# Kernel optimization log

Hardware: AMD Instinct MI355X
Metric: run time of the kernel (lower is better)

The kernel has to match this reference:

```python
import jax, jax.numpy as jnp
import numpy as np

# Tsit5 Butcher tableau (Tsitouras 2011), b7 = 0 for the accepted solution.
_C = (0.161, 0.327, 0.9, 0.9800255409045097, 1.0)
_A = (
    (0.161,),
    (-0.008480655492356989, 0.335480655492357),
    (2.8971530571054935, -6.359448489975075, 4.3622954328695815),
    (5.325864828439257, -11.748883564062828, 7.4955393428898365, -0.09249506636175525),
    (5.86145544294642, -12.92096931784711, 8.159367898576159, -0.071584973281401, -0.028269050394068383),
)
_B = (0.09646076681806523, 0.01, 0.4798896504144996, 1.379008574103742, -3.290069515436081, 2.324710524099774)

K_STEPS, BATCH, N_STATE, N_INPUT, HIDDEN = 512, 64, 128, 32, 256


def setup_inputs() -> dict:
    key = jax.random.key(0)
    k1, k2, k3, k4 = jax.random.split(key, 4)
    ts = jnp.linspace(0.0, 1.0, K_STEPS, dtype=jnp.float32)
    y0 = jax.random.normal(k1, (BATCH, N_STATE), dtype=jnp.float32)
    us = jax.random.normal(k2, (BATCH, K_STEPS, N_INPUT), dtype=jnp.float32)
    fan_in = 1 + N_STATE + N_INPUT  # t, y, u
    W1 = jax.random.normal(k3, (HIDDEN, fan_in), dtype=jnp.float32) / np.sqrt(fan_in)
    b1 = jnp.zeros((HIDDEN,), dtype=jnp.float32)
    W2 = jax.random.normal(k4, (N_STATE, HIDDEN), dtype=jnp.float32) / np.sqrt(HIDDEN)
    b2 = jnp.zeros((N_STATE,), dtype=jnp.float32)
    return {"ts": ts, "y0": y0, "us": us, "W1": W1, "b1": b1, "W2": W2, "b2": b2}


def _solve(ts, y0_i, us_i, W1, b1, W2, b2):
    """Integrate one trajectory with fixed-step Tsit5 on the save grid."""
    dt_grid = jnp.diff(ts)                              # (k-1,)
    # backward-Hermite derivative estimates for the input signal u(t)
    d = jnp.diff(us_i, axis=0) / dt_grid[:, None]       # (k-1, m)
    d = jnp.concatenate([d[:1], d], axis=0)             # (k, m)

    def func(t, y, u):
        z = jnp.concatenate([t[None], y, u])
        return W2 @ jnp.tanh(W1 @ z + b1) + b2

    def u_at(i, theta):
        # cubic Hermite interpolation of u on interval [ts[i], ts[i+1]]
        h = dt_grid[i]
        u0, u1, d0, d1 = us_i[i], us_i[i + 1], d[i], d[i + 1]
        t2 = theta * theta
        t3 = t2 * theta
        return ((2 * t3 - 3 * t2 + 1) * u0 + (t3 - 2 * t2 + theta) * h * d0
                + (-2 * t3 + 3 * t2) * u1 + (t3 - t2) * h * d1)

    def step(y, i):
        t0, h = ts[i], dt_grid[i]
        ks = []
        k = func(t0, y, u_at(i, jnp.float32(0.0)))
        ks.append(k)
        for c, arow in zip(_C, _A):
            ytmp = y + h * sum(a * kj for a, kj in zip(arow, ks))
            ks.append(func(t0 + c * h, ytmp, u_at(i, jnp.float32(c))))
        y_new = y + h * sum(b * kj for b, kj in zip(_B, ks))
        return y_new, y_new

    _, ys = jax.lax.scan(step, y0_i, jnp.arange(ts.shape[0] - 1))
    return jnp.concatenate([y0_i[None], ys], axis=0)    # (k, n)


def reference(ts, y0, us, W1, b1, W2, b2):
    return jax.vmap(_solve, in_axes=(None, 0, 0, None, None, None, None))(
        ts, y0, us, W1, b1, W2, b2
    )
```

## Files before the change

### kernel.cpp

```cpp
#include <hip/hip_runtime.h>

namespace {

typedef _Float16 h2 __attribute__((ext_vector_type(2)));
typedef _Float16 f16x8 __attribute__((ext_vector_type(8)));
typedef float    f32x4 __attribute__((ext_vector_type(4)));

constexpr int KSTEPS = 512;
constexpr int NSTATE = 128;
constexpr int NINPUT = 32;
constexpr int HID    = 256;
constexpr int FANIN  = 161;
constexpr int BATCH  = 64;
constexpr int CHUNK  = 64;
constexpr int NCH    = 8;

constexpr size_t WS_M  = 0;
constexpr size_t WS_C  = WS_M + (size_t)HID * HID * 2;
constexpr size_t WS_US = WS_C + HID * 4;
constexpr size_t WS_HB = WS_US + (size_t)BATCH * KSTEPS * NINPUT * 2;
constexpr size_t WS_T  = WS_HB + (size_t)BATCH * KSTEPS * HID * 2;

__device__ __forceinline__ float fdot2(h2 a, h2 b, float c) {
#if __has_builtin(__builtin_amdgcn_fdot2)
  return __builtin_amdgcn_fdot2(a, b, c, false);
#else
  return c + (float)a[0] * (float)b[0] + (float)a[1] * (float)b[1];
#endif
}

__device__ __forceinline__ float fast_tanh(float x) {
  float e2 = __builtin_amdgcn_exp2f(x * 2.8853900817779268f);
  float r  = __builtin_amdgcn_rcpf(e2 + 1.0f);
  return __builtin_fmaf(-2.0f, r, 1.0f);
}

#define BAR() __asm__ volatile("s_waitcnt lgkmcnt(0)\n\ts_barrier" ::: "memory")

union F4 { float4 f; h2 h[4]; };

__global__ __launch_bounds__(256)
void k1_compose(const float* __restrict__ W1, const float* __restrict__ W2,
                const float* __restrict__ b2, _Float16* __restrict__ wsM,
                float* __restrict__ wsC) {
  const int j  = blockIdx.x;
  const int hc = threadIdx.x;
  const float* w1row = W1 + (size_t)j * FANIN + 1;
  float acc = 0.0f;
  for (int o = 0; o < NSTATE; ++o)
    acc = __builtin_fmaf(w1row[o], W2[(size_t)o * HID + hc], acc);
  wsM[(size_t)j * HID + hc] = (_Float16)acc;
  if (hc == 0) {
    float ca = 0.0f;
    for (int o = 0; o < NSTATE; ++o) ca = __builtin_fmaf(w1row[o], b2[o], ca);
    wsC[j] = ca;
  }
}

__global__ __launch_bounds__(256)
void k1b_transcode(const float* __restrict__ us, _Float16* __restrict__ us16) {
  const size_t idx = ((size_t)blockIdx.x * 256 + threadIdx.x) * 4;
  const float4 v = *(const float4*)(us + idx);
  us16[idx + 0] = (_Float16)v.x;
  us16[idx + 1] = (_Float16)v.y;
  us16[idx + 2] = (_Float16)v.z;
  us16[idx + 3] = (_Float16)v.w;
}

__global__ __launch_bounds__(256)
__attribute__((amdgpu_waves_per_eu(1, 1)))
void k2_main(const float* __restrict__ ts,
             const float* __restrict__ y0,
             const float* __restrict__ W1,
             const float* __restrict__ b1,
             char* __restrict__ ws)
{
  const int lt = threadIdx.x;
  const int w  = lt >> 6;
  const int ln = lt & 63;
  const int klo = ((ln >> 4) & 3) * 8;
  const int j  = 64 * w + 16 * ((ln >> 2) & 3) + 4 * (ln >> 4) + (ln & 3);
  const int b  = blockIdx.x;

  const _Float16* wsM  = (const _Float16*)(ws + WS_M);
  const float*    wsC  = (const float*)(ws + WS_C);
  const _Float16* us16 = (const _Float16*)(ws + WS_US) + (size_t)b * KSTEPS * NINPUT;
  _Float16*       wsHB = (_Float16*)(ws + WS_HB) + (size_t)b * KSTEPS * HID;
  float*          wsT  = (float*)(ws + WS_T) + (size_t)b * NCH * HID;

  __shared__ __align__(16) _Float16 hbuf[2][HID];
  __shared__ __align__(16) float y0s[NSTATE];
  __shared__ __align__(16) float tss[KSTEPS];
  __shared__ __align__(16) _Float16 usl[KSTEPS * NINPUT];

  {
    const F4* src = (const F4*)us16;
    F4* dst = (F4*)usl;
    #pragma unroll
    for (int it = 0; it < 8; ++it) dst[lt + 256 * it] = src[lt + 256 * it];
    tss[lt] = ts[lt];
    tss[lt + 256] = ts[lt + 256];
  }

  f16x8 af[4][8];
  #pragma unroll
  for (int t = 0; t < 4; ++t) {
    const int row = 64 * w + 16 * t + (ln & 15);
    #pragma unroll
    for (int kk = 0; kk < 8; ++kk)
      af[t][kk] = *(const f16x8*)(wsM + (size_t)row * HID + kk * 32 + klo);
  }

  const float* w1row = W1 + (size_t)j * FANIN;
  const float  w1t   = w1row[0];
  h2 w1u[16];
  #pragma unroll
  for (int i = 0; i < 16; ++i)
    w1u[i] = h2{(_Float16)w1row[129 + 2 * i], (_Float16)w1row[130 + 2 * i]};
  const float cR = wsC[j];

  if (lt < NSTATE) y0s[lt] = y0[(size_t)b * NSTATE + lt];
  __syncthreads();
  float P = b1[j];
  {
    const float* wy = w1row + 1;
    #pragma unroll 8
    for (int o = 0; o < NSTATE; ++o) P = __builtin_fmaf(wy[o], y0s[o], P);
  }

  constexpr double CcD[5] = {0.161, 0.327, 0.9, 0.9800255409045097, 1.0};
  constexpr float Af[5][5] = {
    {0.161f, 0.f, 0.f, 0.f, 0.f},
    {-0.008480655492356989f, 0.335480655492357f, 0.f, 0.f, 0.f},
    {2.8971530571054935f, -6.359448489975075f, 4.3622954328695815f, 0.f, 0.f},
    {5.325864828439257f, -11.748883564062828f, 7.4955393428898365f, -0.09249506636175525f, 0.f},
    {5.86145544294642f, -12.92096931784711f, 8.159367898576159f, -0.071584973281401f,
     -0.028269050394068383f}};
  constexpr float Bf[6] = {0.09646076681806523f, 0.01f, 0.4798896504144996f,
                           1.379008574103742f, -3.290069515436081f, 2.324710524099774f};

  float Ua, Ub = 0.0f, Uaprev = 0.0f, D = 0.0f;
  {
    const F4* up = (const F4*)(usl);
    F4 u0 = up[0], u1 = up[1], u2 = up[2], u3 = up[3];
    float s = 0.0f;
    #pragma unroll
    for (int i = 0; i < 4; ++i) {
      s = fdot2(w1u[i],      u0.h[i], s);
      s = fdot2(w1u[4 + i],  u1.h[i], s);
      s = fdot2(w1u[8 + i],  u2.h[i], s);
      s = fdot2(w1u[12 + i], u3.h[i], s);
    }
    Ua = s;
  }

  float tcur = ts[0], tn1 = ts[1];
  float dtp = 1.0f;
  float h0v = fast_tanh(P + Ua + w1t * tcur);
  hbuf[0][j] = (_Float16)h0v;
  float hB = Bf[0] * h0v;
  float Sacc = 0.0f;
  float aR[6];

  for (int i = 0; i < KSTEPS - 1; ++i) {
    const float dt = tn1 - tcur;
    const int   i2 = (i + 2 < KSTEPS) ? (i + 2) : (KSTEPS - 1);
    const float tn2 = tss[i2];
    F4 ur0, ur1, ur2, ur3;
    {
      const F4* up = (const F4*)(&usl[(i + 1) * NINPUT]);
      ur0 = up[0]; ur1 = up[1]; ur2 = up[2]; ur3 = up[3];
    }

    if (i > 0 && (i & (CHUNK - 1)) == 0)
      wsT[(size_t)(i >> 6) * HID + j] = Sacc;

    #pragma unroll
    for (int e = 0; e < 6; ++e) {
      BAR();

      if (e == 5) {
        wsHB[(size_t)i * HID + j] = (_Float16)hB;
      }
      if (e == 0) {
        float s = 0.0f;
        #pragma unroll
        for (int q = 0; q < 4; ++q) {
          s = fdot2(w1u[q],      ur0.h[q], s);
          s = fdot2(w1u[4 + q],  ur1.h[q], s);
          s = fdot2(w1u[8 + q],  ur2.h[q], s);
          s = fdot2(w1u[12 + q], ur3.h[q], s);
        }
        Ub = s;
        D = (i == 0) ? (Ub - Ua)
                     : (Ua - Uaprev) * (dt * __builtin_amdgcn_rcpf(dtp));
      }

      const _Float16* hb = hbuf[e & 1];
      f32x4 ac0 = {0.f, 0.f, 0.f, 0.f};
      f32x4 ac1 = {0.f, 0.f, 0.f, 0.f};
      f32x4 ac2 = {0.f, 0.f, 0.f, 0.f};
      f32x4 ac3 = {0.f, 0.f, 0.f, 0.f};
      #pragma unroll
      for (int kk = 0; kk < 8; ++kk) {
        const f16x8 bf = *(const f16x8*)(hb + kk * 32 + klo);
        ac0 = __builtin_amdgcn_mfma_f32_16x16x32_f16(af[0][kk], bf, ac0, 0, 0, 0);
        ac1 = __builtin_amdgcn_mfma_f32_16x16x32_f16(af[1][kk], bf, ac1, 0, 0, 0);
        ac2 = __builtin_amdgcn_mfma_f32_16x16x32_f16(af[2][kk], bf, ac2, 0, 0, 0);
        ac3 = __builtin_amdgcn_mfma_f32_16x16x32_f16(af[3][kk], bf, ac3, 0, 0, 0);
      }
      float ae;
      {
        const bool b0 = (ln & 1) != 0;
        const bool b1s = (ln & 2) != 0;
        float e0 = b1s ? (b0 ? ac0[3] : ac0[2]) : (b0 ? ac0[1] : ac0[0]);
        float e1 = b1s ? (b0 ? ac1[3] : ac1[2]) : (b0 ? ac1[1] : ac1[0]);
        float e2 = b1s ? (b0 ? ac2[3] : ac2[2]) : (b0 ? ac2[1] : ac2[0]);
        float e3 = b1s ? (b0 ? ac3[3] : ac3[2]) : (b0 ? ac3[1] : ac3[0]);
        const bool t0 = (ln & 4) != 0;
        const bool t1 = (ln & 8) != 0;
        ae = t1 ? (t0 ? e3 : e2) : (t0 ? e1 : e0);
      }
      ae += cR;
      aR[e] = ae;

      if (e < 5) {
        float acm = 0.0f;
        #pragma unroll
        for (int mm = 0; mm <= e; ++mm) acm = __builtin_fmaf(Af[e][mm], aR[mm], acm);
        const double th = CcD[e];
        const float cu0 = (float)(th * th * th - 2.0 * th * th + 1.0);
        const float cu1 = (float)(2.0 * th * th - th * th * th);
        const float cd0 = (float)(th * th * th - 2.0 * th * th + th);
        const float ut  = cu0 * Ua + cu1 * Ub + cd0 * D;
        const float te  = __builtin_fmaf((float)th, dt, tcur);
        float pre = __builtin_fmaf(dt, acm, P) + ut;
        pre = __builtin_fmaf(w1t, te, pre);
        const float hv = fast_tanh(pre);
        hbuf[(e + 1) & 1][j] = (_Float16)hv;
        hB = __builtin_fmaf(Bf[e + 1], hv, hB);
      } else {
        float acm = 0.0f;
        #pragma unroll
        for (int mm = 0; mm < 6; ++mm) acm = __builtin_fmaf(Bf[mm], aR[mm], acm);
        P = __builtin_fmaf(dt, acm, P);
        Sacc = __builtin_fmaf(dt, hB, Sacc);
        float pre = P + Ub;
        pre = __builtin_fmaf(w1t, tn1, pre);
        const float hv = fast_tanh(pre);
        hbuf[0][j] = (_Float16)hv;
        hB = Bf[0] * hv;
      }
    }

    Uaprev = Ua; Ua = Ub;
    dtp = dt; tcur = tn1; tn1 = tn2;
  }
}

__global__ __launch_bounds__(256, 1)
void k4_out(const float* __restrict__ ts,
            const float* __restrict__ y0,
            const float* __restrict__ W2,
            const char* __restrict__ ws,
            float* __restrict__ out)
{
  const int blk = blockIdx.x;
  const int b = blk >> 3;
  const int c = blk & 7;
  const int lt = threadIdx.x;
  const int o    = lt >> 1;
  const int half = lt & 1;

  const _Float16* wsHB = (const _Float16*)(ws + WS_HB) + (size_t)b * KSTEPS * HID;
  const float*    wsT  = (const float*)(ws + WS_T) + (size_t)b * NCH * HID;
  float* outb = out + (size_t)b * KSTEPS * NSTATE;

  __shared__ __align__(16) _Float16 Sb[HID];

  h2 w2r[64];
  {
    const float* row = W2 + (size_t)o * HID + 128 * half;
    #pragma unroll
    for (int i = 0; i < 64; ++i)
      w2r[i] = h2{(_Float16)row[2 * i], (_Float16)row[2 * i + 1]};
  }
  const float y0o = y0[(size_t)b * NSTATE + o];
  if (c == 0 && lt < NSTATE) outb[lt] = y0[(size_t)b * NSTATE + lt];

  float S = (c > 0) ? wsT[(size_t)c * HID + lt] : 0.0f;
  const int i0 = c * CHUNK;
  const int n  = (KSTEPS - 1 - i0 < CHUNK) ? (KSTEPS - 1 - i0) : CHUNK;

  float tc = ts[i0], tn = ts[i0 + 1];
  float hcur = (float)wsHB[(size_t)i0 * HID + lt];
  for (int l = 0; l < n; ++l) {
    const int i = i0 + l;
    const int inx = (i + 1 < KSTEPS - 1) ? (i + 1) : (KSTEPS - 2);
    const float hnext = (float)wsHB[(size_t)inx * HID + lt];
    const float tnn = ts[(i + 2 < KSTEPS) ? (i + 2) : (KSTEPS - 1)];

    const float dt = tn - tc;
    S = __builtin_fmaf(dt, hcur, S);
    Sb[lt] = (_Float16)S;
    __syncthreads();

    const F4* sp = (const F4*)(&Sb[128 * half]);
    float v0 = 0.0f, v1 = 0.0f;
    #pragma unroll
    for (int q = 0; q < 16; ++q) {
      F4 sc = sp[q];
      v0 = fdot2(w2r[4 * q + 0], sc.h[0], v0);
      v1 = fdot2(w2r[4 * q + 1], sc.h[1], v1);
      v0 = fdot2(w2r[4 * q + 2], sc.h[2], v0);
      v1 = fdot2(w2r[4 * q + 3], sc.h[3], v1);
    }
    float v = v0 + v1;
    v += __shfl_xor(v, 1);
    if (half == 0) outb[(size_t)(i + 1) * NSTATE + o] = y0o + v;
    __syncthreads();

    hcur = hnext; tc = tn; tn = tnn;
  }
}

}

extern "C" void kernel_launch(void* const* d_in, const int* in_sizes, int n_in,
                              void* d_out, int out_size, void* d_ws, size_t ws_size,
                              hipStream_t stream) {
  const float* ts = (const float*)d_in[0];
  const float* y0 = (const float*)d_in[1];
  const float* us = (const float*)d_in[2];
  const float* W1 = (const float*)d_in[3];
  const float* b1 = (const float*)d_in[4];
  const float* W2 = (const float*)d_in[5];
  const float* b2 = (const float*)d_in[6];
  float* out = (float*)d_out;
  char* ws = (char*)d_ws;

  _Float16* wsM  = (_Float16*)(ws + WS_M);
  float*    wsC  = (float*)(ws + WS_C);
  _Float16* us16 = (_Float16*)(ws + WS_US);

  hipLaunchKernelGGL(k1_compose, dim3(HID), dim3(HID), 0, stream, W1, W2, b2, wsM, wsC);
  hipLaunchKernelGGL(k1b_transcode, dim3(BATCH * KSTEPS * NINPUT / 1024), dim3(256),
                     0, stream, us, us16);
  hipLaunchKernelGGL(k2_main, dim3(BATCH), dim3(256), 0, stream, ts, y0, W1, b1, ws);
  hipLaunchKernelGGL(k4_out, dim3(BATCH * NCH), dim3(256), 0, stream, ts, y0, W2,
                     (const char*)ws, out);
}
```

Measured before the change: 1.546 ms.

## Split k2_main GEMV across 8 waves with redundant lane pairs per row

Runs the per-trajectory recurrent kernel with 512 threads (8 waves) instead of 256. Each wave now owns 32 hidden rows, issuing two MFMA tiles per kk step instead of four. The output-to-lane mapping is rearranged so each hidden unit is computed by two lanes, and only one of them writes to LDS and global memory. The aim is to shorten the serial MFMA chain per stage, at the cost of more threads doing duplicate scalar tanh work and more waves taking part in each barrier.

```diff
diff --git a/kernel.cpp b/kernel.cpp
--- a/kernel.cpp
+++ b/kernel.cpp
@@ -67,8 +67,8 @@
   us16[idx + 3] = (_Float16)v.w;
 }
 
-__global__ __launch_bounds__(256)
-__attribute__((amdgpu_waves_per_eu(1, 1)))
+__global__ __launch_bounds__(512)
+__attribute__((amdgpu_waves_per_eu(2, 2)))
 void k2_main(const float* __restrict__ ts,
              const float* __restrict__ y0,
              const float* __restrict__ W1,
@@ -78,8 +78,11 @@
   const int lt = threadIdx.x;
   const int w  = lt >> 6;
   const int ln = lt & 63;
-  const int klo = ((ln >> 4) & 3) * 8;
-  const int j  = 64 * w + 16 * ((ln >> 2) & 3) + 4 * (ln >> 4) + (ln & 3);
+  const int c  = ln & 15;
+  const int q  = (ln >> 4) & 3;
+  const int klo = q * 8;
+  const int j  = 32 * w + 16 * (c & 1) + 4 * q + ((c >> 1) & 3);
+  const bool wrl = (c < 8);
   const int b  = blockIdx.x;
 
   const _Float16* wsM  = (const _Float16*)(ws + WS_M);
@@ -97,15 +100,14 @@
     const F4* src = (const F4*)us16;
     F4* dst = (F4*)usl;
     #pragma unroll
-    for (int it = 0; it < 8; ++it) dst[lt + 256 * it] = src[lt + 256 * it];
+    for (int it = 0; it < 4; ++it) dst[lt + 512 * it] = src[lt + 512 * it];
     tss[lt] = ts[lt];
-    tss[lt + 256] = ts[lt + 256];
-  }
-
-  f16x8 af[4][8];
+  }
+
+  f16x8 af[2][8];
   #pragma unroll
-  for (int t = 0; t < 4; ++t) {
-    const int row = 64 * w + 16 * t + (ln & 15);
+  for (int t = 0; t < 2; ++t) {
+    const int row = 32 * w + 16 * t + (ln & 15);
     #pragma unroll
     for (int kk = 0; kk < 8; ++kk)
       af[t][kk] = *(const f16x8*)(wsM + (size_t)row * HID + kk * 32 + klo);
@@ -157,7 +159,7 @@
   float tcur = ts[0], tn1 = ts[1];
   float dtp = 1.0f;
   float h0v = fast_tanh(P + Ua + w1t * tcur);
-  hbuf[0][j] = (_Float16)h0v;
+  if (wrl) hbuf[0][j] = (_Float16)h0v;
   float hB = Bf[0] * h0v;
   float Sacc = 0.0f;
   float aR[6];
@@ -172,24 +174,24 @@
       ur0 = up[0]; ur1 = up[1]; ur2 = up[2]; ur3 = up[3];
     }
 
-    if (i > 0 && (i & (CHUNK - 1)) == 0)
+    if (i > 0 && (i & (CHUNK - 1)) == 0 && wrl)
       wsT[(size_t)(i >> 6) * HID + j] = Sacc;
 
     #pragma unroll
     for (int e = 0; e < 6; ++e) {
       BAR();
 
-      if (e == 5) {
+      if (e == 5 && wrl) {
         wsHB[(size_t)i * HID + j] = (_Float16)hB;
       }
       if (e == 0) {
         float s = 0.0f;
         #pragma unroll
-        for (int q = 0; q < 4; ++q) {
-          s = fdot2(w1u[q],      ur0.h[q], s);
-          s = fdot2(w1u[4 + q],  ur1.h[q], s);
-          s = fdot2(w1u[8 + q],  ur2.h[q], s);
-          s = fdot2(w1u[12 + q], ur3.h[q], s);
+        for (int qq = 0; qq < 4; ++qq) {
+          s = fdot2(w1u[qq],      ur0.h[qq], s);
+          s = fdot2(w1u[4 + qq],  ur1.h[qq], s);
+          s = fdot2(w1u[8 + qq],  ur2.h[qq], s);
+          s = fdot2(w1u[12 + qq], ur3.h[qq], s);
         }
         Ub = s;
         D = (i == 0) ? (Ub - Ua)
@@ -199,27 +201,22 @@
       const _Float16* hb = hbuf[e & 1];
       f32x4 ac0 = {0.f, 0.f, 0.f, 0.f};
       f32x4 ac1 = {0.f, 0.f, 0.f, 0.f};
-      f32x4 ac2 = {0.f, 0.f, 0.f, 0.f};
-      f32x4 ac3 = {0.f, 0.f, 0.f, 0.f};
       #pragma unroll
       for (int kk = 0; kk < 8; ++kk) {
         const f16x8 bf = *(const f16x8*)(hb + kk * 32 + klo);
         ac0 = __builtin_amdgcn_mfma_f32_16x16x32_f16(af[0][kk], bf, ac0, 0, 0, 0);
         ac1 = __builtin_amdgcn_mfma_f32_16x16x32_f16(af[1][kk], bf, ac1, 0, 0, 0);
-        ac2 = __builtin_amdgcn_mfma_f32_16x16x32_f16(af[2][kk], bf, ac2, 0, 0, 0);
-        ac3 = __builtin_amdgcn_mfma_f32_16x16x32_f16(af[3][kk], bf, ac3, 0, 0, 0);
       }
       float ae;
       {
-        const bool b0 = (ln & 1) != 0;
-        const bool b1s = (ln & 2) != 0;
-        float e0 = b1s ? (b0 ? ac0[3] : ac0[2]) : (b0 ? ac0[1] : ac0[0]);
-        float e1 = b1s ? (b0 ? ac1[3] : ac1[2]) : (b0 ? ac1[1] : ac1[0]);
-        float e2 = b1s ? (b0 ? ac2[3] : ac2[2]) : (b0 ? ac2[1] : ac2[0]);
-        float e3 = b1s ? (b0 ? ac3[3] : ac3[2]) : (b0 ? ac3[1] : ac3[0]);
-        const bool t0 = (ln & 4) != 0;
-        const bool t1 = (ln & 8) != 0;
-        ae = t1 ? (t0 ? e3 : e2) : (t0 ? e1 : e0);
+        const bool tsel = (c & 1) != 0;
+        float v0 = tsel ? ac1[0] : ac0[0];
+        float v1 = tsel ? ac1[1] : ac0[1];
+        float v2 = tsel ? ac1[2] : ac0[2];
+        float v3 = tsel ? ac1[3] : ac0[3];
+        const bool r0 = (c & 2) != 0;
+        const bool r1 = (c & 4) != 0;
+        ae = r1 ? (r0 ? v3 : v2) : (r0 ? v1 : v0);
       }
       ae += cR;
       aR[e] = ae;
@@ -237,7 +234,7 @@
         float pre = __builtin_fmaf(dt, acm, P) + ut;
         pre = __builtin_fmaf(w1t, te, pre);
         const float hv = fast_tanh(pre);
-        hbuf[(e + 1) & 1][j] = (_Float16)hv;
+        if (wrl) hbuf[(e + 1) & 1][j] = (_Float16)hv;
         hB = __builtin_fmaf(Bf[e + 1], hv, hB);
       } else {
         float acm = 0.0f;
@@ -248,7 +245,7 @@
         float pre = P + Ub;
         pre = __builtin_fmaf(w1t, tn1, pre);
         const float hv = fast_tanh(pre);
-        hbuf[0][j] = (_Float16)hv;
+        if (wrl) hbuf[0][j] = (_Float16)hv;
         hB = Bf[0] * hv;
       }
     }
@@ -346,7 +343,7 @@
   hipLaunchKernelGGL(k1_compose, dim3(HID), dim3(HID), 0, stream, W1, W2, b2, wsM, wsC);
   hipLaunchKernelGGL(k1b_transcode, dim3(BATCH * KSTEPS * NINPUT / 1024), dim3(256),
                      0, stream, us, us16);
-  hipLaunchKernelGGL(k2_main, dim3(BATCH), dim3(256), 0, stream, ts, y0, W1, b1, ws);
+  hipLaunchKernelGGL(k2_main, dim3(BATCH), dim3(512), 0, stream, ts, y0, W1, b1, ws);
   hipLaunchKernelGGL(k4_out, dim3(BATCH * NCH), dim3(256), 0, stream, ts, y0, W2,
                      (const char*)ws, out);
 }
```

After: 1.591 ms. 1.03x slower.

## Pair two trajectories per block and ping-pong MFMA with scalar stage tails

Applied to the files above, without the earlier changes.

k2_main now runs two batch trajectories per 512-thread block, two waves per SIMD, and launches half as many blocks. The groups are staggered by half a stage: while one group runs the MFMA matvec for the current RK stage, the other computes its tanh/Hermite tail, with a barrier between the phases. The lagging group keeps its hidden state in a register and writes it to shared memory just before its own MFMA. The aim is to hide the serial scalar tail latency behind the other trajectory's matrix work. The cost is two barriers per stage instead of one, and half as many CUs in use.

```diff
diff --git a/kernel.cpp b/kernel.cpp
--- a/kernel.cpp
+++ b/kernel.cpp
@@ -67,20 +67,22 @@
   us16[idx + 3] = (_Float16)v.w;
 }
 
-__global__ __launch_bounds__(256)
-__attribute__((amdgpu_waves_per_eu(1, 1)))
+__global__ __launch_bounds__(512)
+__attribute__((amdgpu_waves_per_eu(2, 2)))
 void k2_main(const float* __restrict__ ts,
              const float* __restrict__ y0,
              const float* __restrict__ W1,
              const float* __restrict__ b1,
              char* __restrict__ ws)
 {
-  const int lt = threadIdx.x;
-  const int w  = lt >> 6;
-  const int ln = lt & 63;
+  const int lt  = threadIdx.x;
+  const int tg  = lt >> 8;
+  const int ltg = lt & 255;
+  const int w   = ltg >> 6;
+  const int ln  = ltg & 63;
   const int klo = ((ln >> 4) & 3) * 8;
-  const int j  = 64 * w + 16 * ((ln >> 2) & 3) + 4 * (ln >> 4) + (ln & 3);
-  const int b  = blockIdx.x;
+  const int j   = 64 * w + 16 * ((ln >> 2) & 3) + 4 * (ln >> 4) + (ln & 3);
+  const int b   = blockIdx.x * 2 + tg;
 
   const _Float16* wsM  = (const _Float16*)(ws + WS_M);
   const float*    wsC  = (const float*)(ws + WS_C);
@@ -88,18 +90,17 @@
   _Float16*       wsHB = (_Float16*)(ws + WS_HB) + (size_t)b * KSTEPS * HID;
   float*          wsT  = (float*)(ws + WS_T) + (size_t)b * NCH * HID;
 
-  __shared__ __align__(16) _Float16 hbuf[2][HID];
-  __shared__ __align__(16) float y0s[NSTATE];
+  __shared__ __align__(16) _Float16 hbuf[2][2][HID];
+  __shared__ __align__(16) float y0s[2][NSTATE];
   __shared__ __align__(16) float tss[KSTEPS];
-  __shared__ __align__(16) _Float16 usl[KSTEPS * NINPUT];
+  __shared__ __align__(16) _Float16 usl[2][KSTEPS * NINPUT];
 
   {
     const F4* src = (const F4*)us16;
-    F4* dst = (F4*)usl;
-    #pragma unroll
-    for (int it = 0; it < 8; ++it) dst[lt + 256 * it] = src[lt + 256 * it];
+    F4* dst = (F4*)usl[tg];
+    #pragma unroll
+    for (int it = 0; it < 8; ++it) dst[ltg + 256 * it] = src[ltg + 256 * it];
     tss[lt] = ts[lt];
-    tss[lt + 256] = ts[lt + 256];
   }
 
   f16x8 af[4][8];
@@ -119,13 +120,13 @@
     w1u[i] = h2{(_Float16)w1row[129 + 2 * i], (_Float16)w1row[130 + 2 * i]};
   const float cR = wsC[j];
 
-  if (lt < NSTATE) y0s[lt] = y0[(size_t)b * NSTATE + lt];
+  if (ltg < NSTATE) y0s[tg][ltg] = y0[(size_t)b * NSTATE + ltg];
   __syncthreads();
   float P = b1[j];
   {
     const float* wy = w1row + 1;
     #pragma unroll 8
-    for (int o = 0; o < NSTATE; ++o) P = __builtin_fmaf(wy[o], y0s[o], P);
+    for (int o = 0; o < NSTATE; ++o) P = __builtin_fmaf(wy[o], y0s[tg][o], P);
   }
 
   constexpr double CcD[5] = {0.161, 0.327, 0.9, 0.9800255409045097, 1.0};
@@ -141,7 +142,7 @@
 
   float Ua, Ub = 0.0f, Uaprev = 0.0f, D = 0.0f;
   {
-    const F4* up = (const F4*)(usl);
+    const F4* up = (const F4*)(usl[tg]);
     F4 u0 = up[0], u1 = up[1], u2 = up[2], u3 = up[3];
     float s = 0.0f;
     #pragma unroll
@@ -157,10 +158,89 @@
   float tcur = ts[0], tn1 = ts[1];
   float dtp = 1.0f;
   float h0v = fast_tanh(P + Ua + w1t * tcur);
-  hbuf[0][j] = (_Float16)h0v;
+  if (tg == 0) hbuf[0][0][j] = (_Float16)h0v;
+  float hreg = h0v;
   float hB = Bf[0] * h0v;
   float Sacc = 0.0f;
   float aR[6];
+  __syncthreads();
+
+  #define READ_MFMA(EB)                                                        \
+    {                                                                          \
+      const _Float16* hb = hbuf[tg][EB];                                       \
+      f32x4 ac0 = {0.f, 0.f, 0.f, 0.f};                                        \
+      f32x4 ac1 = {0.f, 0.f, 0.f, 0.f};                                        \
+      f32x4 ac2 = {0.f, 0.f, 0.f, 0.f};                                        \
+      f32x4 ac3 = {0.f, 0.f, 0.f, 0.f};                                        \
+      _Pragma("unroll")                                                        \
+      for (int kk = 0; kk < 8; ++kk) {                                         \
+        const f16x8 bf = *(const f16x8*)(hb + kk * 32 + klo);                  \
+        ac0 = __builtin_amdgcn_mfma_f32_16x16x32_f16(af[0][kk], bf, ac0, 0, 0, 0); \
+        ac1 = __builtin_amdgcn_mfma_f32_16x16x32_f16(af[1][kk], bf, ac1, 0, 0, 0); \
+        ac2 = __builtin_amdgcn_mfma_f32_16x16x32_f16(af[2][kk], bf, ac2, 0, 0, 0); \
+        ac3 = __builtin_amdgcn_mfma_f32_16x16x32_f16(af[3][kk], bf, ac3, 0, 0, 0); \
+      }                                                                        \
+      const bool b0 = (ln & 1) != 0;                                           \
+      const bool b1s = (ln & 2) != 0;                                          \
+      float e0 = b1s ? (b0 ? ac0[3] : ac0[2]) : (b0 ? ac0[1] : ac0[0]);        \
+      float e1 = b1s ? (b0 ? ac1[3] : ac1[2]) : (b0 ? ac1[1] : ac1[0]);        \
+      float e2 = b1s ? (b0 ? ac2[3] : ac2[2]) : (b0 ? ac2[1] : ac2[0]);        \
+      float e3 = b1s ? (b0 ? ac3[3] : ac3[2]) : (b0 ? ac3[1] : ac3[0]);        \
+      const bool t0 = (ln & 4) != 0;                                           \
+      const bool t1 = (ln & 8) != 0;                                           \
+      ae = t1 ? (t0 ? e3 : e2) : (t0 ? e1 : e0);                               \
+    }
+
+  #define TAIL(E, DO_W)                                                        \
+    {                                                                          \
+      if ((E) == 0) {                                                          \
+        float s = 0.0f;                                                        \
+        _Pragma("unroll")                                                      \
+        for (int qq = 0; qq < 4; ++qq) {                                       \
+          s = fdot2(w1u[qq],      ur0.h[qq], s);                               \
+          s = fdot2(w1u[4 + qq],  ur1.h[qq], s);                               \
+          s = fdot2(w1u[8 + qq],  ur2.h[qq], s);                               \
+          s = fdot2(w1u[12 + qq], ur3.h[qq], s);                               \
+        }                                                                      \
+        Ub = s;                                                                \
+        D = (i == 0) ? (Ub - Ua)                                               \
+                     : (Ua - Uaprev) * (dt * __builtin_amdgcn_rcpf(dtp));      \
+      }                                                                        \
+      ae += cR;                                                                \
+      aR[(E)] = ae;                                                            \
+      if ((E) < 5) {                                                           \
+        float acm = 0.0f;                                                      \
+        _Pragma("unroll")                                                      \
+        for (int mm = 0; mm <= (E); ++mm)                                      \
+          acm = __builtin_fmaf(Af[(E)][mm], aR[mm], acm);                      \
+        const double th = CcD[(E)];                                            \
+        const float cu0 = (float)(th * th * th - 2.0 * th * th + 1.0);         \
+        const float cu1 = (float)(2.0 * th * th - th * th * th);               \
+        const float cd0 = (float)(th * th * th - 2.0 * th * th + th);          \
+        const float ut  = cu0 * Ua + cu1 * Ub + cd0 * D;                       \
+        const float te  = __builtin_fmaf((float)th, dt, tcur);                 \
+        float pre = __builtin_fmaf(dt, acm, P) + ut;                           \
+        pre = __builtin_fmaf(w1t, te, pre);                                    \
+        const float hv = fast_tanh(pre);                                       \
+        if (DO_W) hbuf[tg][((E) + 1) & 1][j] = (_Float16)hv;                   \
+        else      hreg = hv;                                                   \
+        hB = __builtin_fmaf(Bf[(E) + 1], hv, hB);                              \
+      } else {                                                                 \
+        wsHB[(size_t)i * HID + j] = (_Float16)hB;                              \
+        float acm = 0.0f;                                                      \
+        _Pragma("unroll")                                                      \
+        for (int mm = 0; mm < 6; ++mm)                                         \
+          acm = __builtin_fmaf(Bf[mm], aR[mm], acm);                           \
+        P = __builtin_fmaf(dt, acm, P);                                        \
+        Sacc = __builtin_fmaf(dt, hB, Sacc);                                   \
+        float pre = P + Ub;                                                    \
+        pre = __builtin_fmaf(w1t, tn1, pre);                                   \
+        const float hv = fast_tanh(pre);                                       \
+        if (DO_W) hbuf[tg][0][j] = (_Float16)hv;                               \
+        else      hreg = hv;                                                   \
+        hB = Bf[0] * hv;                                                       \
+      }                                                                        \
+    }
 
   for (int i = 0; i < KSTEPS - 1; ++i) {
     const float dt = tn1 - tcur;
@@ -168,7 +248,7 @@
     const float tn2 = tss[i2];
     F4 ur0, ur1, ur2, ur3;
     {
-      const F4* up = (const F4*)(&usl[(i + 1) * NINPUT]);
+      const F4* up = (const F4*)(&usl[tg][(i + 1) * NINPUT]);
       ur0 = up[0]; ur1 = up[1]; ur2 = up[2]; ur3 = up[3];
     }
 
@@ -177,85 +257,29 @@
 
     #pragma unroll
     for (int e = 0; e < 6; ++e) {
+      float ae;
+      if (tg == 0) {
+        READ_MFMA(e & 1);
+      } else {
+        hbuf[1][e & 1][j] = (_Float16)hreg;
+      }
       BAR();
-
-      if (e == 5) {
-        wsHB[(size_t)i * HID + j] = (_Float16)hB;
+      if (tg == 0) {
+        TAIL(e, 1);
+      } else {
+        READ_MFMA(e & 1);
       }
-      if (e == 0) {
-        float s = 0.0f;
-        #pragma unroll
-        for (int q = 0; q < 4; ++q) {
-          s = fdot2(w1u[q],      ur0.h[q], s);
-          s = fdot2(w1u[4 + q],  ur1.h[q], s);
-          s = fdot2(w1u[8 + q],  ur2.h[q], s);
-          s = fdot2(w1u[12 + q], ur3.h[q], s);
-        }
-        Ub = s;
-        D = (i == 0) ? (Ub - Ua)
-                     : (Ua - Uaprev) * (dt * __builtin_amdgcn_rcpf(dtp));
-      }
-
-      const _Float16* hb = hbuf[e & 1];
-      f32x4 ac0 = {0.f, 0.f, 0.f, 0.f};
-      f32x4 ac1 = {0.f, 0.f, 0.f, 0.f};
-      f32x4 ac2 = {0.f, 0.f, 0.f, 0.f};
-      f32x4 ac3 = {0.f, 0.f, 0.f, 0.f};
-      #pragma unroll
-      for (int kk = 0; kk < 8; ++kk) {
-        const f16x8 bf = *(const f16x8*)(hb + kk * 32 + klo);
-        ac0 = __builtin_amdgcn_mfma_f32_16x16x32_f16(af[0][kk], bf, ac0, 0, 0, 0);
-        ac1 = __builtin_amdgcn_mfma_f32_16x16x32_f16(af[1][kk], bf, ac1, 0, 0, 0);
-        ac2 = __builtin_amdgcn_mfma_f32_16x16x32_f16(af[2][kk], bf, ac2, 0, 0, 0);
-        ac3 = __builtin_amdgcn_mfma_f32_16x16x32_f16(af[3][kk], bf, ac3, 0, 0, 0);
-      }
-      float ae;
-      {
-        const bool b0 = (ln & 1) != 0;
-        const bool b1s = (ln & 2) != 0;
-        float e0 = b1s ? (b0 ? ac0[3] : ac0[2]) : (b0 ? ac0[1] : ac0[0]);
-        float e1 = b1s ? (b0 ? ac1[3] : ac1[2]) : (b0 ? ac1[1] : ac1[0]);
-        float e2 = b1s ? (b0 ? ac2[3] : ac2[2]) : (b0 ? ac2[1] : ac2[0]);
-        float e3 = b1s ? (b0 ? ac3[3] : ac3[2]) : (b0 ? ac3[1] : ac3[0]);
-        const bool t0 = (ln & 4) != 0;
-        const bool t1 = (ln & 8) != 0;
-        ae = t1 ? (t0 ? e3 : e2) : (t0 ? e1 : e0);
-      }
-      ae += cR;
-      aR[e] = ae;
-
-      if (e < 5) {
-        float acm = 0.0f;
-        #pragma unroll
-        for (int mm = 0; mm <= e; ++mm) acm = __builtin_fmaf(Af[e][mm], aR[mm], acm);
-        const double th = CcD[e];
-        const float cu0 = (float)(th * th * th - 2.0 * th * th + 1.0);
-        const float cu1 = (float)(2.0 * th * th - th * th * th);
-        const float cd0 = (float)(th * th * th - 2.0 * th * th + th);
-        const float ut  = cu0 * Ua + cu1 * Ub + cd0 * D;
-        const float te  = __builtin_fmaf((float)th, dt, tcur);
-        float pre = __builtin_fmaf(dt, acm, P) + ut;
-        pre = __builtin_fmaf(w1t, te, pre);
-        const float hv = fast_tanh(pre);
-        hbuf[(e + 1) & 1][j] = (_Float16)hv;
-        hB = __builtin_fmaf(Bf[e + 1], hv, hB);
-      } else {
-        float acm = 0.0f;
-        #pragma unroll
-        for (int mm = 0; mm < 6; ++mm) acm = __builtin_fmaf(Bf[mm], aR[mm], acm);
-        P = __builtin_fmaf(dt, acm, P);
-        Sacc = __builtin_fmaf(dt, hB, Sacc);
-        float pre = P + Ub;
-        pre = __builtin_fmaf(w1t, tn1, pre);
-        const float hv = fast_tanh(pre);
-        hbuf[0][j] = (_Float16)hv;
-        hB = Bf[0] * hv;
+      BAR();
+      if (tg == 1) {
+        TAIL(e, 0);
       }
     }
 
     Uaprev = Ua; Ua = Ub;
     dtp = dt; tcur = tn1; tn1 = tn2;
   }
+  #undef READ_MFMA
+  #undef TAIL
 }
 
 __global__ __launch_bounds__(256, 1)
@@ -346,7 +370,7 @@
   hipLaunchKernelGGL(k1_compose, dim3(HID), dim3(HID), 0, stream, W1, W2, b2, wsM, wsC);
   hipLaunchKernelGGL(k1b_transcode, dim3(BATCH * KSTEPS * NINPUT / 1024), dim3(256),
                      0, stream, us, us16);
-  hipLaunchKernelGGL(k2_main, dim3(BATCH), dim3(256), 0, stream, ts, y0, W1, b1, ws);
+  hipLaunchKernelGGL(k2_main, dim3(BATCH / 2), dim3(512), 0, stream, ts, y0, W1, b1, ws);
   hipLaunchKernelGGL(k4_out, dim3(BATCH * NCH), dim3(256), 0, stream, ts, y0, W2,
                      (const char*)ws, out);
 }
```

Measured after the change: 2.684 ms. 1.74x slower.
